# Kernel optimization log

Hardware: AMD Instinct MI355X
Metric: run time of the kernel (lower is better)

Reference implementation:

```python
import jax, jax.numpy as jnp
import numpy as np

C, E, H, TOPK = 768, 8, 3072, 2
B, T = 2048, 1

def setup_inputs() -> dict:
    key = jax.random.key(0)
    ks = jax.random.split(key, 5)
    proj_std = 0.02 * (2 * 12) ** (-0.5)  # n_layer = 12
    return {
        "x": jax.random.normal(ks[0], (B, T, C), jnp.float32),
        "w_router": 0.02 * jax.random.normal(ks[1], (C, E), jnp.float32),
        "w_c_fc": 0.02 * jax.random.normal(ks[2], (E, C, H), jnp.float32),
        "b_c_fc": jnp.zeros((E, 1, H), jnp.float32),
        "w_gate": 0.02 * jax.random.normal(ks[3], (E, C, H), jnp.float32),
        "b_gate": jnp.zeros((E, 1, H), jnp.float32),
        "w_c_proj": proj_std * jax.random.normal(ks[4], (E, H, C), jnp.float32),
        "b_c_proj": jnp.zeros((E, 1, C), jnp.float32),
        "top_k": TOPK,
    }

def reference(x, w_router, w_c_fc, b_c_fc, w_gate, b_gate, w_c_proj, b_c_proj, top_k):
    Bx, Tx, Cx = x.shape
    n_experts = w_c_fc.shape[0]
    xf = x.reshape(-1, Cx)                      # (N, C), N = B*T
    N = xf.shape[0]
    logits = xf @ w_router                      # (N, E); router has no bias (mlp_bias=False)
    top_k_logits, expert_indices = jax.lax.top_k(logits, top_k)   # (N, k)
    # put_along_axis into -inf, then softmax -> sparse routing probs
    sparse = jnp.full_like(logits, -jnp.inf)
    sparse = sparse.at[jnp.arange(N)[:, None], expert_indices].set(top_k_logits)
    expert_probs = jax.nn.softmax(sparse, axis=-1)                # (N, E)
    # dispatch: per-expert running position of each selected token
    mask = jax.nn.one_hot(expert_indices, n_experts, axis=-1).sum(axis=1)  # (N, E)
    positions = jnp.cumsum(mask, axis=0) * mask                   # (N, E)
    cap = top_k * Bx  # NOTE: module uses B (pre-flatten), not B*T
    ee, tt = jnp.nonzero(positions.T, size=cap)                   # expert id, token id
    pos = positions.T[ee, tt].astype(jnp.int32) - 1               # slot within expert buffer
    expert_inputs = jnp.zeros((n_experts, cap, Cx), x.dtype)
    expert_inputs = expert_inputs.at[ee, pos].set(xf[tt])         # (E, cap, C)
    # per-expert SwiGLU MLP (grouped GEMMs)
    h = jnp.einsum('eti,eih->eth', expert_inputs, w_c_fc) + b_c_fc
    g = jax.nn.silu(jnp.einsum('eti,eih->eth', expert_inputs, w_gate) + b_gate)
    o = jnp.einsum('eth,eho->eto', h * g, w_c_proj) + b_c_proj    # (E, cap, C)
    # combine: weighted scatter-add back to token order
    y = jnp.zeros_like(xf)
    y = y.at[tt].add(o[ee, pos] * expert_probs[tt, ee][:, None])  # (N, C)
    return y
```

## Files before the change

kernel.cpp:

```cpp
#include <hip/hip_runtime.h>
#include <hip/hip_bf16.h>
#include <cmath>

#define C_DIM 768
#define E_DIM 8
#define H_DIM 3072
#define CNT_STRIDE 32

typedef short s16x8 __attribute__((ext_vector_type(8)));
typedef short s16x4 __attribute__((ext_vector_type(4)));
typedef float f32x4 __attribute__((ext_vector_type(4)));

__device__ __forceinline__ float bf2f(unsigned short u) {
  unsigned int v = ((unsigned int)u) << 16;
  float f;
  __builtin_memcpy(&f, &v, 4);
  return f;
}

__device__ __forceinline__ unsigned short f2bf(float f) {
  __hip_bfloat16 h = __float2bfloat16(f);
  unsigned short u;
  __builtin_memcpy(&u, &h, 2);
  return u;
}

__global__ void tr_cvt_kernel(const float* __restrict__ in, unsigned short* __restrict__ out,
                              int R, int CC) {
  const int e = blockIdx.z;
  const int c0 = blockIdx.x * 64;
  const int r0 = blockIdx.y * 64;
  const int tid = threadIdx.x;
  __shared__ unsigned short T[64 * 68];
  const int row = tid >> 2;
  const int cq = (tid & 3) * 4;
  const float* src = in + (size_t)e * R * CC + (size_t)(r0 + row) * CC + c0;
#pragma unroll
  for (int j = 0; j < 4; ++j) {
    const int c = cq + j * 16;
    const float4 v = *(const float4*)(src + c);
    T[(c + 0) * 68 + row] = f2bf(v.x);
    T[(c + 1) * 68 + row] = f2bf(v.y);
    T[(c + 2) * 68 + row] = f2bf(v.z);
    T[(c + 3) * 68 + row] = f2bf(v.w);
  }
  __syncthreads();
  const int oc = tid >> 2;
  const int half = (tid & 3) * 16;
  unsigned short* dst = out + (size_t)e * CC * R + (size_t)(c0 + oc) * R + r0 + half;
  *(uint4*)(dst) = *(const uint4*)(&T[oc * 68 + half]);
  *(uint4*)(dst + 8) = *(const uint4*)(&T[oc * 68 + half + 8]);
}

__global__ void router_kernel(const float* __restrict__ x,
                              const float* __restrict__ w_r,
                              int* __restrict__ tok_e,
                              float* __restrict__ tok_p) {
  const int t = blockIdx.x;
  const int lane = threadIdx.x;
  float acc[E_DIM];
#pragma unroll
  for (int e = 0; e < E_DIM; ++e) acc[e] = 0.f;
  for (int c = lane; c < C_DIM; c += 64) {
    const float xv = x[(size_t)t * C_DIM + c];
    const float4 w0 = *(const float4*)(w_r + (size_t)c * E_DIM);
    const float4 w1 = *(const float4*)(w_r + (size_t)c * E_DIM + 4);
    acc[0] += xv * w0.x; acc[1] += xv * w0.y; acc[2] += xv * w0.z; acc[3] += xv * w0.w;
    acc[4] += xv * w1.x; acc[5] += xv * w1.y; acc[6] += xv * w1.z; acc[7] += xv * w1.w;
  }
#pragma unroll
  for (int e = 0; e < E_DIM; ++e) {
#pragma unroll
    for (int off = 32; off > 0; off >>= 1) acc[e] += __shfl_xor(acc[e], off, 64);
  }
  if (lane == 0) {
    int i0 = 0;
#pragma unroll
    for (int e = 1; e < E_DIM; ++e)
      if (acc[e] > acc[i0]) i0 = e;
    int i1 = (i0 == 0) ? 1 : 0;
#pragma unroll
    for (int e = 0; e < E_DIM; ++e)
      if (e != i0 && acc[e] > acc[i1]) i1 = e;
    const float d = expf(acc[i1] - acc[i0]);
    const float p0 = 1.f / (1.f + d);
    tok_e[2 * t] = i0;
    tok_e[2 * t + 1] = i1;
    tok_p[2 * t] = p0;
    tok_p[2 * t + 1] = 1.f - p0;
  }
}

__global__ void assign_kernel(const int* __restrict__ tok_e,
                              int* __restrict__ counts,
                              int* __restrict__ tok_rank,
                              int N) {
  __shared__ int lcnt[E_DIM];
  __shared__ int lbase[E_DIM];
  const int tid = threadIdx.x;
  const int t = blockIdx.x * blockDim.x + tid;
  if (tid < E_DIM) lcnt[tid] = 0;
  __syncthreads();
  int e0 = 0, e1 = 0, r0 = 0, r1 = 0;
  const bool valid = (t < N);
  if (valid) {
    e0 = tok_e[2 * t];
    e1 = tok_e[2 * t + 1];
    r0 = atomicAdd(&lcnt[e0], 1);
    r1 = atomicAdd(&lcnt[e1], 1);
  }
  __syncthreads();
  if (tid < E_DIM) lbase[tid] = atomicAdd(counts + tid * CNT_STRIDE, lcnt[tid]);
  __syncthreads();
  if (valid) {
    tok_rank[2 * t] = lbase[e0] + r0;
    tok_rank[2 * t + 1] = lbase[e1] + r1;
  }
}

__global__ void schedule_kernel(const int* __restrict__ counts,
                                int* __restrict__ pad_off,
                                int* __restrict__ table_e,
                                int* __restrict__ table_row,
                                int tableCap) {
  if (threadIdx.x != 0) return;
  int running = 0, idx = 0;
  for (int e = 0; e < E_DIM; ++e) {
    pad_off[e] = running;
    const int tiles = (counts[e * CNT_STRIDE] + 127) >> 7;
    for (int j = 0; j < tiles && idx < tableCap; ++j) {
      table_e[idx] = e;
      table_row[idx] = running + j * 128;
      ++idx;
    }
    running += tiles << 7;
  }
  for (; idx < tableCap; ++idx) table_e[idx] = -1;
}

__global__ void gather_kernel(const float* __restrict__ x,
                              const int* __restrict__ tok_e,
                              const int* __restrict__ tok_rank,
                              const int* __restrict__ pad_off,
                              int* __restrict__ tok_slot,
                              unsigned short* __restrict__ Xg) {
  const int t = blockIdx.x;
  const int lane = threadIdx.x;
  const int s0 = pad_off[tok_e[2 * t]] + tok_rank[2 * t];
  const int s1 = pad_off[tok_e[2 * t + 1]] + tok_rank[2 * t + 1];
  if (lane == 0) {
    tok_slot[2 * t] = s0;
    tok_slot[2 * t + 1] = s1;
  }
  const float4* src = (const float4*)(x + (size_t)t * C_DIM);
  for (int q = lane; q < C_DIM / 4; q += 64) {
    const float4 v = src[q];
    s16x4 p;
    p[0] = (short)f2bf(v.x);
    p[1] = (short)f2bf(v.y);
    p[2] = (short)f2bf(v.z);
    p[3] = (short)f2bf(v.w);
    *(s16x4*)(Xg + (size_t)s0 * C_DIM + q * 4) = p;
    *(s16x4*)(Xg + (size_t)s1 * C_DIM + q * 4) = p;
  }
}

__global__ __launch_bounds__(256, 2) void fcgate_kernel(
    const unsigned short* __restrict__ Xg, const unsigned short* __restrict__ wfcT,
    const float* __restrict__ b_fc, const unsigned short* __restrict__ wgtT,
    const float* __restrict__ b_gt, const int* __restrict__ table_e,
    const int* __restrict__ table_row, unsigned short* __restrict__ act) {
  const int mt = blockIdx.y;
  const int e = table_e[mt];
  if (e < 0) return;
  const int row0 = table_row[mt];
  const int nt = blockIdx.x;
  const int tid = threadIdx.x;
  const int lane = tid & 63;
  const int wid = tid >> 6;
  const int quad = lane >> 4;
  const int l16 = lane & 15;
  const int wrow = (wid >> 1) * 64;
  const int wcol = (wid & 1) * 64;

  __shared__ unsigned short As[128 * 40];
  __shared__ unsigned short BsF[128 * 40];
  __shared__ unsigned short BsG[128 * 40];

  const unsigned short* pF = wfcT + (size_t)e * H_DIM * C_DIM + (size_t)(nt * 128) * C_DIM;
  const unsigned short* pG = wgtT + (size_t)e * H_DIM * C_DIM + (size_t)(nt * 128) * C_DIM;

  f32x4 accH[4][4], accG[4][4];
#pragma unroll
  for (int i = 0; i < 4; ++i)
#pragma unroll
    for (int j = 0; j < 4; ++j)
#pragma unroll
      for (int r = 0; r < 4; ++r) {
        accH[i][j][r] = 0.f;
        accG[i][j][r] = 0.f;
      }

  const int sr = tid >> 1;
  const int sc = (tid & 1) * 16;

  for (int k0 = 0; k0 < C_DIM; k0 += 32) {
    const uint4 av0 = *(const uint4*)(Xg + (size_t)(row0 + sr) * C_DIM + k0 + sc);
    const uint4 av1 = *(const uint4*)(Xg + (size_t)(row0 + sr) * C_DIM + k0 + sc + 8);
    const uint4 bf0 = *(const uint4*)(pF + (size_t)sr * C_DIM + k0 + sc);
    const uint4 bf1 = *(const uint4*)(pF + (size_t)sr * C_DIM + k0 + sc + 8);
    const uint4 bg0 = *(const uint4*)(pG + (size_t)sr * C_DIM + k0 + sc);
    const uint4 bg1 = *(const uint4*)(pG + (size_t)sr * C_DIM + k0 + sc + 8);
    __syncthreads();
    *(uint4*)(&As[sr * 40 + sc]) = av0;
    *(uint4*)(&As[sr * 40 + sc + 8]) = av1;
    *(uint4*)(&BsF[sr * 40 + sc]) = bf0;
    *(uint4*)(&BsF[sr * 40 + sc + 8]) = bf1;
    *(uint4*)(&BsG[sr * 40 + sc]) = bg0;
    *(uint4*)(&BsG[sr * 40 + sc + 8]) = bg1;
    __syncthreads();

    s16x8 a[4], bF[4], bG[4];
#pragma unroll
    for (int tr = 0; tr < 4; ++tr)
      a[tr] = *(const s16x8*)(&As[(wrow + tr * 16 + l16) * 40 + quad * 8]);
#pragma unroll
    for (int tc = 0; tc < 4; ++tc)
      bF[tc] = *(const s16x8*)(&BsF[(wcol + tc * 16 + l16) * 40 + quad * 8]);
#pragma unroll
    for (int tc = 0; tc < 4; ++tc)
      bG[tc] = *(const s16x8*)(&BsG[(wcol + tc * 16 + l16) * 40 + quad * 8]);

#pragma unroll
    for (int tr = 0; tr < 4; ++tr)
#pragma unroll
      for (int tc = 0; tc < 4; ++tc) {
        accH[tr][tc] = __builtin_amdgcn_mfma_f32_16x16x32_bf16(a[tr], bF[tc], accH[tr][tc], 0, 0, 0);
        accG[tr][tc] = __builtin_amdgcn_mfma_f32_16x16x32_bf16(a[tr], bG[tc], accG[tr][tc], 0, 0, 0);
      }
  }

#pragma unroll
  for (int tc = 0; tc < 4; ++tc) {
    const int col = nt * 128 + wcol + tc * 16 + l16;
    const float bf = b_fc[e * H_DIM + col];
    const float bg = b_gt[e * H_DIM + col];
#pragma unroll
    for (int tr = 0; tr < 4; ++tr) {
#pragma unroll
      for (int r = 0; r < 4; ++r) {
        const int row = row0 + wrow + tr * 16 + quad * 4 + r;
        const float hv = accH[tr][tc][r] + bf;
        const float gv = accG[tr][tc][r] + bg;
        const float sv = gv / (1.f + __expf(-gv));
        act[(size_t)row * H_DIM + col] = f2bf(hv * sv);
      }
    }
  }
}

__global__ __launch_bounds__(256, 2) void proj_kernel(
    const unsigned short* __restrict__ act, const unsigned short* __restrict__ wpjT,
    const float* __restrict__ b_pj, const int* __restrict__ table_e,
    const int* __restrict__ table_row, float* __restrict__ o) {
  const int mt = blockIdx.y;
  const int e = table_e[mt];
  if (e < 0) return;
  const int row0 = table_row[mt];
  const int nt = blockIdx.x;
  const int tid = threadIdx.x;
  const int lane = tid & 63;
  const int wid = tid >> 6;
  const int quad = lane >> 4;
  const int l16 = lane & 15;
  const int wrow = (wid >> 1) * 64;
  const int wcol = (wid & 1) * 32;

  __shared__ unsigned short As[128 * 40];
  __shared__ unsigned short Bs[64 * 40];

  const unsigned short* pB = wpjT + (size_t)e * C_DIM * H_DIM + (size_t)(nt * 64) * H_DIM;

  f32x4 acc[4][2];
#pragma unroll
  for (int i = 0; i < 4; ++i)
#pragma unroll
    for (int j = 0; j < 2; ++j)
#pragma unroll
      for (int r = 0; r < 4; ++r) acc[i][j][r] = 0.f;

  const int sr = tid >> 1;
  const int sc = (tid & 1) * 16;
  const int br = tid >> 2;
  const int bc = (tid & 3) * 8;

  for (int k0 = 0; k0 < H_DIM; k0 += 32) {
    const uint4 av0 = *(const uint4*)(act + (size_t)(row0 + sr) * H_DIM + k0 + sc);
    const uint4 av1 = *(const uint4*)(act + (size_t)(row0 + sr) * H_DIM + k0 + sc + 8);
    const uint4 bv = *(const uint4*)(pB + (size_t)br * H_DIM + k0 + bc);
    __syncthreads();
    *(uint4*)(&As[sr * 40 + sc]) = av0;
    *(uint4*)(&As[sr * 40 + sc + 8]) = av1;
    *(uint4*)(&Bs[br * 40 + bc]) = bv;
    __syncthreads();

    s16x8 a[4], bB[2];
#pragma unroll
    for (int tr = 0; tr < 4; ++tr)
      a[tr] = *(const s16x8*)(&As[(wrow + tr * 16 + l16) * 40 + quad * 8]);
#pragma unroll
    for (int tc = 0; tc < 2; ++tc)
      bB[tc] = *(const s16x8*)(&Bs[(wcol + tc * 16 + l16) * 40 + quad * 8]);

#pragma unroll
    for (int tr = 0; tr < 4; ++tr)
#pragma unroll
      for (int tc = 0; tc < 2; ++tc)
        acc[tr][tc] = __builtin_amdgcn_mfma_f32_16x16x32_bf16(a[tr], bB[tc], acc[tr][tc], 0, 0, 0);
  }

#pragma unroll
  for (int tc = 0; tc < 2; ++tc) {
    const int col = nt * 64 + wcol + tc * 16 + l16;
    const float bp = b_pj[e * C_DIM + col];
#pragma unroll
    for (int tr = 0; tr < 4; ++tr) {
#pragma unroll
      for (int r = 0; r < 4; ++r) {
        const int row = row0 + wrow + tr * 16 + quad * 4 + r;
        o[(size_t)row * C_DIM + col] = acc[tr][tc][r] + bp;
      }
    }
  }
}

__global__ void combine_kernel(const float* __restrict__ o,
                               const int* __restrict__ tok_slot,
                               const float* __restrict__ tok_p,
                               float* __restrict__ out) {
  const int t = blockIdx.x;
  const int lane = threadIdx.x;
  const int s0 = tok_slot[2 * t], s1 = tok_slot[2 * t + 1];
  const float p0 = tok_p[2 * t], p1 = tok_p[2 * t + 1];
  const f32x4* r0 = (const f32x4*)(o + (size_t)s0 * C_DIM);
  const f32x4* r1 = (const f32x4*)(o + (size_t)s1 * C_DIM);
  f32x4* dst = (f32x4*)(out + (size_t)t * C_DIM);
  for (int q = lane; q < C_DIM / 4; q += 64) {
    const f32x4 a = r0[q];
    const f32x4 b = r1[q];
    dst[q] = a * p0 + b * p1;
  }
}

extern "C" void kernel_launch(void* const* d_in, const int* in_sizes, int n_in,
                              void* d_out, int out_size, void* d_ws, size_t ws_size,
                              hipStream_t stream) {
  const int N = in_sizes[0] / C_DIM;
  char* ws = (char*)d_ws;

  int* counts = (int*)(ws + 0);
  int* pad_off = (int*)(ws + 1024);
  int* table_e = (int*)(ws + 1152);
  int* table_row = (int*)(ws + 1408);
  int* tok_e = (int*)(ws + 2048);
  float* tok_p = (float*)(ws + 2048 + (size_t)8 * N);
  int* tok_rank = (int*)(ws + 2048 + (size_t)16 * N);
  int* tok_slot = (int*)(ws + 2048 + (size_t)24 * N);

  int tableCap = (2 * N) / 128 + E_DIM;
  if (tableCap > 64) tableCap = 64;

  size_t off = 2048 + (size_t)32 * N;
  off = (off + 255) & ~(size_t)255;
  const size_t R = (size_t)2 * N + 128 * E_DIM;
  unsigned short* Xg = (unsigned short*)(ws + off);
  const size_t xg_bytes = R * C_DIM * 2;

  const size_t wbytes = (size_t)E_DIM * C_DIM * H_DIM * 2;
  size_t wfc_off = (off + xg_bytes + 255) & ~(size_t)255;
  size_t wgt_off = wfc_off + wbytes;
  size_t wpj_off = wgt_off + wbytes;
  unsigned short* wfcT = (unsigned short*)(ws + wfc_off);
  unsigned short* wgtT = (unsigned short*)(ws + wgt_off);
  unsigned short* wpjT = (unsigned short*)(ws + wpj_off);

  size_t act_off = (wpj_off + wbytes + 255) & ~(size_t)255;
  unsigned short* act = (unsigned short*)(ws + act_off);
  size_t o_off = (act_off + R * H_DIM * 2 + 255) & ~(size_t)255;
  float* o = (float*)(ws + o_off);
  const size_t need = o_off + R * C_DIM * 4;
  if (ws_size < need || n_in < 9) return;

  hipMemsetAsync(ws, 0, 2048, stream);
  hipMemsetAsync(Xg, 0, xg_bytes, stream);

  tr_cvt_kernel<<<dim3(H_DIM / 64, C_DIM / 64, E_DIM), 256, 0, stream>>>(
      (const float*)d_in[2], wfcT, C_DIM, H_DIM);
  tr_cvt_kernel<<<dim3(H_DIM / 64, C_DIM / 64, E_DIM), 256, 0, stream>>>(
      (const float*)d_in[4], wgtT, C_DIM, H_DIM);
  tr_cvt_kernel<<<dim3(C_DIM / 64, H_DIM / 64, E_DIM), 256, 0, stream>>>(
      (const float*)d_in[6], wpjT, H_DIM, C_DIM);

  router_kernel<<<N, 64, 0, stream>>>((const float*)d_in[0], (const float*)d_in[1],
                                      tok_e, tok_p);
  assign_kernel<<<(N + 255) / 256, 256, 0, stream>>>(tok_e, counts, tok_rank, N);
  schedule_kernel<<<1, 64, 0, stream>>>(counts, pad_off, table_e, table_row, tableCap);
  gather_kernel<<<N, 64, 0, stream>>>((const float*)d_in[0], tok_e, tok_rank, pad_off,
                                      tok_slot, Xg);
  fcgate_kernel<<<dim3(H_DIM / 128, tableCap), 256, 0, stream>>>(
      Xg, wfcT, (const float*)d_in[3], wgtT, (const float*)d_in[5],
      table_e, table_row, act);
  proj_kernel<<<dim3(C_DIM / 64, tableCap), 256, 0, stream>>>(
      act, wpjT, (const float*)d_in[7], table_e, table_row, o);
  combine_kernel<<<N, 64, 0, stream>>>(o, tok_slot, tok_p, (float*)d_out);
}
```

Measured before the change: 414.5 us.

## Double-buffer GEMM tiles with direct global-to-LDS loads in both expert GEMMs

```diff
diff --git a/kernel.cpp b/kernel.cpp
--- a/kernel.cpp
+++ b/kernel.cpp
@@ -23,6 +23,12 @@
   unsigned short u;
   __builtin_memcpy(&u, &h, 2);
   return u;
+}
+
+__device__ __forceinline__ void gll16(const unsigned short* g, unsigned short* l) {
+  __builtin_amdgcn_global_load_lds(
+      (const __attribute__((address_space(1))) void*)g,
+      (__attribute__((address_space(3))) void*)l, 16, 0, 0);
 }
 
 __global__ void tr_cvt_kernel(const float* __restrict__ in, unsigned short* __restrict__ out,
@@ -183,12 +189,14 @@
   const int wrow = (wid >> 1) * 64;
   const int wcol = (wid & 1) * 64;
 
-  __shared__ unsigned short As[128 * 40];
-  __shared__ unsigned short BsF[128 * 40];
-  __shared__ unsigned short BsG[128 * 40];
-
-  const unsigned short* pF = wfcT + (size_t)e * H_DIM * C_DIM + (size_t)(nt * 128) * C_DIM;
-  const unsigned short* pG = wgtT + (size_t)e * H_DIM * C_DIM + (size_t)(nt * 128) * C_DIM;
+  __shared__ __align__(16) unsigned short L[2][3 * 4096];
+
+  const int srow = wid * 32 + (lane >> 2);
+  const int scol = (lane & 3) * 8;
+  const unsigned short* gA = Xg + (size_t)(row0 + srow) * C_DIM + scol;
+  const unsigned short* gF = wfcT + (size_t)e * H_DIM * C_DIM + (size_t)(nt * 128 + srow) * C_DIM + scol;
+  const unsigned short* gG = wgtT + (size_t)e * H_DIM * C_DIM + (size_t)(nt * 128 + srow) * C_DIM + scol;
+  const int ldsOff = wid * 1024;
 
   f32x4 accH[4][4], accG[4][4];
 #pragma unroll
@@ -201,36 +209,32 @@
         accG[i][j][r] = 0.f;
       }
 
-  const int sr = tid >> 1;
-  const int sc = (tid & 1) * 16;
-
-  for (int k0 = 0; k0 < C_DIM; k0 += 32) {
-    const uint4 av0 = *(const uint4*)(Xg + (size_t)(row0 + sr) * C_DIM + k0 + sc);
-    const uint4 av1 = *(const uint4*)(Xg + (size_t)(row0 + sr) * C_DIM + k0 + sc + 8);
-    const uint4 bf0 = *(const uint4*)(pF + (size_t)sr * C_DIM + k0 + sc);
-    const uint4 bf1 = *(const uint4*)(pF + (size_t)sr * C_DIM + k0 + sc + 8);
-    const uint4 bg0 = *(const uint4*)(pG + (size_t)sr * C_DIM + k0 + sc);
-    const uint4 bg1 = *(const uint4*)(pG + (size_t)sr * C_DIM + k0 + sc + 8);
-    __syncthreads();
-    *(uint4*)(&As[sr * 40 + sc]) = av0;
-    *(uint4*)(&As[sr * 40 + sc + 8]) = av1;
-    *(uint4*)(&BsF[sr * 40 + sc]) = bf0;
-    *(uint4*)(&BsF[sr * 40 + sc + 8]) = bf1;
-    *(uint4*)(&BsG[sr * 40 + sc]) = bg0;
-    *(uint4*)(&BsG[sr * 40 + sc + 8]) = bg1;
-    __syncthreads();
-
+  auto stage = [&](int buf, int k0) {
+    unsigned short* As = &L[buf][0];
+    unsigned short* BF = &L[buf][4096];
+    unsigned short* BG = &L[buf][8192];
+    gll16(gA + k0, As + ldsOff);
+    gll16(gA + 16 * C_DIM + k0, As + ldsOff + 512);
+    gll16(gF + k0, BF + ldsOff);
+    gll16(gF + 16 * C_DIM + k0, BF + ldsOff + 512);
+    gll16(gG + k0, BG + ldsOff);
+    gll16(gG + 16 * C_DIM + k0, BG + ldsOff + 512);
+  };
+
+  auto compute = [&](int buf) {
+    const unsigned short* As = &L[buf][0];
+    const unsigned short* BF = &L[buf][4096];
+    const unsigned short* BG = &L[buf][8192];
     s16x8 a[4], bF[4], bG[4];
 #pragma unroll
     for (int tr = 0; tr < 4; ++tr)
-      a[tr] = *(const s16x8*)(&As[(wrow + tr * 16 + l16) * 40 + quad * 8]);
+      a[tr] = *(const s16x8*)(As + (wrow + tr * 16 + l16) * 32 + quad * 8);
 #pragma unroll
     for (int tc = 0; tc < 4; ++tc)
-      bF[tc] = *(const s16x8*)(&BsF[(wcol + tc * 16 + l16) * 40 + quad * 8]);
+      bF[tc] = *(const s16x8*)(BF + (wcol + tc * 16 + l16) * 32 + quad * 8);
 #pragma unroll
     for (int tc = 0; tc < 4; ++tc)
-      bG[tc] = *(const s16x8*)(&BsG[(wcol + tc * 16 + l16) * 40 + quad * 8]);
-
+      bG[tc] = *(const s16x8*)(BG + (wcol + tc * 16 + l16) * 32 + quad * 8);
 #pragma unroll
     for (int tr = 0; tr < 4; ++tr)
 #pragma unroll
@@ -238,7 +242,25 @@
         accH[tr][tc] = __builtin_amdgcn_mfma_f32_16x16x32_bf16(a[tr], bF[tc], accH[tr][tc], 0, 0, 0);
         accG[tr][tc] = __builtin_amdgcn_mfma_f32_16x16x32_bf16(a[tr], bG[tc], accG[tr][tc], 0, 0, 0);
       }
-  }
+  };
+
+  stage(0, 0);
+  int buf = 0;
+  for (int i = 0; i < 23; ++i) {
+    stage(buf ^ 1, (i + 1) * 32);
+    asm volatile("s_waitcnt vmcnt(6)" ::: "memory");
+    __builtin_amdgcn_s_barrier();
+    asm volatile("" ::: "memory");
+    compute(buf);
+    asm volatile("" ::: "memory");
+    __builtin_amdgcn_s_barrier();
+    asm volatile("" ::: "memory");
+    buf ^= 1;
+  }
+  asm volatile("s_waitcnt vmcnt(0)" ::: "memory");
+  __builtin_amdgcn_s_barrier();
+  asm volatile("" ::: "memory");
+  compute(buf);
 
 #pragma unroll
   for (int tc = 0; tc < 4; ++tc) {
@@ -259,7 +281,7 @@
   }
 }
 
-__global__ __launch_bounds__(256, 2) void proj_kernel(
+__global__ __launch_bounds__(256, 4) void proj_kernel(
     const unsigned short* __restrict__ act, const unsigned short* __restrict__ wpjT,
     const float* __restrict__ b_pj, const int* __restrict__ table_e,
     const int* __restrict__ table_row, float* __restrict__ o) {
@@ -276,10 +298,13 @@
   const int wrow = (wid >> 1) * 64;
   const int wcol = (wid & 1) * 32;
 
-  __shared__ unsigned short As[128 * 40];
-  __shared__ unsigned short Bs[64 * 40];
-
-  const unsigned short* pB = wpjT + (size_t)e * C_DIM * H_DIM + (size_t)(nt * 64) * H_DIM;
+  __shared__ __align__(16) unsigned short L[2][4096 + 2048];
+
+  const int srowA = wid * 32 + (lane >> 2);
+  const int srowB = wid * 16 + (lane >> 2);
+  const int scol = (lane & 3) * 8;
+  const unsigned short* gA = act + (size_t)(row0 + srowA) * H_DIM + scol;
+  const unsigned short* gB = wpjT + (size_t)e * C_DIM * H_DIM + (size_t)(nt * 64 + srowB) * H_DIM + scol;
 
   f32x4 acc[4][2];
 #pragma unroll
@@ -289,35 +314,48 @@
 #pragma unroll
       for (int r = 0; r < 4; ++r) acc[i][j][r] = 0.f;
 
-  const int sr = tid >> 1;
-  const int sc = (tid & 1) * 16;
-  const int br = tid >> 2;
-  const int bc = (tid & 3) * 8;
-
-  for (int k0 = 0; k0 < H_DIM; k0 += 32) {
-    const uint4 av0 = *(const uint4*)(act + (size_t)(row0 + sr) * H_DIM + k0 + sc);
-    const uint4 av1 = *(const uint4*)(act + (size_t)(row0 + sr) * H_DIM + k0 + sc + 8);
-    const uint4 bv = *(const uint4*)(pB + (size_t)br * H_DIM + k0 + bc);
-    __syncthreads();
-    *(uint4*)(&As[sr * 40 + sc]) = av0;
-    *(uint4*)(&As[sr * 40 + sc + 8]) = av1;
-    *(uint4*)(&Bs[br * 40 + bc]) = bv;
-    __syncthreads();
-
+  auto stage = [&](int buf, int k0) {
+    unsigned short* As = &L[buf][0];
+    unsigned short* Bs = &L[buf][4096];
+    gll16(gA + k0, As + wid * 1024);
+    gll16(gA + 16 * H_DIM + k0, As + wid * 1024 + 512);
+    gll16(gB + k0, Bs + wid * 512);
+  };
+
+  auto compute = [&](int buf) {
+    const unsigned short* As = &L[buf][0];
+    const unsigned short* Bs = &L[buf][4096];
     s16x8 a[4], bB[2];
 #pragma unroll
     for (int tr = 0; tr < 4; ++tr)
-      a[tr] = *(const s16x8*)(&As[(wrow + tr * 16 + l16) * 40 + quad * 8]);
+      a[tr] = *(const s16x8*)(As + (wrow + tr * 16 + l16) * 32 + quad * 8);
 #pragma unroll
     for (int tc = 0; tc < 2; ++tc)
-      bB[tc] = *(const s16x8*)(&Bs[(wcol + tc * 16 + l16) * 40 + quad * 8]);
-
+      bB[tc] = *(const s16x8*)(Bs + (wcol + tc * 16 + l16) * 32 + quad * 8);
 #pragma unroll
     for (int tr = 0; tr < 4; ++tr)
 #pragma unroll
       for (int tc = 0; tc < 2; ++tc)
         acc[tr][tc] = __builtin_amdgcn_mfma_f32_16x16x32_bf16(a[tr], bB[tc], acc[tr][tc], 0, 0, 0);
-  }
+  };
+
+  stage(0, 0);
+  int buf = 0;
+  for (int i = 0; i < 95; ++i) {
+    stage(buf ^ 1, (i + 1) * 32);
+    asm volatile("s_waitcnt vmcnt(3)" ::: "memory");
+    __builtin_amdgcn_s_barrier();
+    asm volatile("" ::: "memory");
+    compute(buf);
+    asm volatile("" ::: "memory");
+    __builtin_amdgcn_s_barrier();
+    asm volatile("" ::: "memory");
+    buf ^= 1;
+  }
+  asm volatile("s_waitcnt vmcnt(0)" ::: "memory");
+  __builtin_amdgcn_s_barrier();
+  asm volatile("" ::: "memory");
+  compute(buf);
 
 #pragma unroll
   for (int tc = 0; tc < 2; ++tc) {
```

Result: faster. 391.3 us (-5.6%).
